# Kernel tuning notes

Measured on AMD Instinct MI355X. Metric: run time of the kernel, lower is better.

The kernel has to match this reference:

```python
import jax, jax.numpy as jnp
import numpy as np

B, M = 64, 2048
D_LLM = 4096
D_T, D_P, D_C = 256, 512, 1024
NH_T, NH_P, NH_C = 4, 8, 16
S_T, S_P, S_C = 4, 8, 4
LN_EPS = 1e-5


def setup_inputs() -> dict:
    key = jax.random.key(0)
    ks = iter(jax.random.split(key, 48))
    def n(shape, s=0.02):
        return jax.random.normal(next(ks), shape, jnp.float32) * s
    inp = {
        "hidden_state": jax.random.normal(next(ks), (B, D_LLM), jnp.float32),
        "time_fiber": jax.random.normal(next(ks), (M, D_T), jnp.float32),
        "topic_fiber": jax.random.normal(next(ks), (M, D_P), jnp.float32),
        "ctx_fiber": jax.random.normal(next(ks), (M, D_C), jnp.float32),
        "mem_mask": jnp.zeros((B, M), bool),
        # BundleQueryHeads: Linear(d_LLM -> d_F_*) per bundle (torch weight layout (out,in))
        "Wq_time": n((D_T, D_LLM)), "bq_time": jnp.zeros((D_T,), jnp.float32),
        "Wq_topic": n((D_P, D_LLM)), "bq_topic": jnp.zeros((D_P,), jnp.float32),
        "Wq_ctx": n((D_C, D_LLM)), "bq_ctx": jnp.zeros((D_C,), jnp.float32),
        # nn.MultiheadAttention packed in_proj (3d, d) and out_proj (d, d)
        "Wqkv_time": n((3 * D_T, D_T)), "bqkv_time": jnp.zeros((3 * D_T,), jnp.float32),
        "Wo_time": n((D_T, D_T)), "bo_time": jnp.zeros((D_T,), jnp.float32),
        "Wqkv_topic": n((3 * D_P, D_P)), "bqkv_topic": jnp.zeros((3 * D_P,), jnp.float32),
        "Wo_topic": n((D_P, D_P)), "bo_topic": jnp.zeros((D_P,), jnp.float32),
        "Wqkv_ctx": n((3 * D_C, D_C)), "bqkv_ctx": jnp.zeros((3 * D_C,), jnp.float32),
        "Wo_ctx": n((D_C, D_C)), "bo_ctx": jnp.zeros((D_C,), jnp.float32),
        # per-slot lifts stacked: (slots, d_F, d_LLM) for einsum 'bd,sde->bse'
        "Wlift_time": n((S_T, D_T, D_LLM)), "blift_time": jnp.zeros((S_T, D_LLM), jnp.float32),
        "Wlift_topic": n((S_P, D_P, D_LLM)), "blift_topic": jnp.zeros((S_P, D_LLM), jnp.float32),
        "Wlift_ctx": n((S_C, D_C, D_LLM)), "blift_ctx": jnp.zeros((S_C, D_LLM), jnp.float32),
        "ln_g": jnp.ones((D_LLM,), jnp.float32),
        "ln_b": jnp.zeros((D_LLM,), jnp.float32),
    }
    return inp


def _mha1(q, kv, Wqkv, bqkv, Wo, bo, nh, mask):
    """Single-query-token MHA. q: (B,d); kv: (M,d) shared across batch; mask: (B,M) True=ignore."""
    d = q.shape[-1]
    hd = d // nh
    Wq, Wk, Wv = jnp.split(Wqkv, 3, axis=0)
    bq, bk, bv = jnp.split(bqkv, 3, axis=0)
    qp = (q @ Wq.T + bq).reshape(-1, nh, hd)    # (B,h,hd)
    kp = (kv @ Wk.T + bk).reshape(-1, nh, hd)   # (M,h,hd)
    vp = (kv @ Wv.T + bv).reshape(-1, nh, hd)   # (M,h,hd)
    scale = 1.0 / np.float32(np.sqrt(hd))
    scores = jnp.einsum('bhd,mhd->bhm', qp, kp) * scale  # (B,h,M)
    scores = jnp.where(mask[:, None, :], jnp.float32(-1e9), scores)
    attn = jax.nn.softmax(scores, axis=-1)
    out = jnp.einsum('bhm,mhd->bhd', attn, vp).reshape(-1, d)  # (B,d)
    return out @ Wo.T + bo


def _layernorm(x, g, b):
    mu = jnp.mean(x, axis=-1, keepdims=True)
    var = jnp.mean((x - mu) ** 2, axis=-1, keepdims=True)
    return (x - mu) * jax.lax.rsqrt(var + LN_EPS) * g + b


def reference(hidden_state, time_fiber, topic_fiber, ctx_fiber, mem_mask,
              Wq_time, bq_time, Wq_topic, bq_topic, Wq_ctx, bq_ctx,
              Wqkv_time, bqkv_time, Wo_time, bo_time,
              Wqkv_topic, bqkv_topic, Wo_topic, bo_topic,
              Wqkv_ctx, bqkv_ctx, Wo_ctx, bo_ctx,
              Wlift_time, blift_time, Wlift_topic, blift_topic, Wlift_ctx, blift_ctx,
              ln_g, ln_b):
    # bundle query heads
    q_time = hidden_state @ Wq_time.T + bq_time
    q_topic = hidden_state @ Wq_topic.T + bq_topic
    q_ctx = hidden_state @ Wq_ctx.T + bq_ctx
    # three single-token cross attentions
    o_time = _mha1(q_time, time_fiber, Wqkv_time, bqkv_time, Wo_time, bo_time, NH_T, mem_mask)
    o_topic = _mha1(q_topic, topic_fiber, Wqkv_topic, bqkv_topic, Wo_topic, bo_topic, NH_P, mem_mask)
    o_ctx = _mha1(q_ctx, ctx_fiber, Wqkv_ctx, bqkv_ctx, Wo_ctx, bo_ctx, NH_C, mem_mask)
    # per-slot lifts, batched across slots
    slots_time = jnp.einsum('bd,sde->bse', o_time, Wlift_time) + blift_time[None]
    slots_topic = jnp.einsum('bd,sde->bse', o_topic, Wlift_topic) + blift_topic[None]
    slots_ctx = jnp.einsum('bd,sde->bse', o_ctx, Wlift_ctx) + blift_ctx[None]
    prefix = jnp.concatenate([slots_time, slots_topic, slots_ctx], axis=1)  # (B, L_mem, d_LLM)
    return _layernorm(prefix, ln_g, ln_b)
```

## Files before the change

kernel.cpp:

```cpp
#include <hip/hip_runtime.h>
#include <cstdint>
#include <cstddef>

typedef __attribute__((ext_vector_type(8))) short short8;
typedef __attribute__((ext_vector_type(4))) float floatx4;

__device__ __forceinline__ unsigned short f2bf(float f) {
    unsigned int u = __builtin_bit_cast(unsigned int, f);
    u += 0x7fffu + ((u >> 16) & 1u);
    return (unsigned short)(u >> 16);
}
__device__ __forceinline__ short8 pack8(float4 a, float4 b) {
    short8 r;
    r[0] = (short)f2bf(a.x); r[1] = (short)f2bf(a.y);
    r[2] = (short)f2bf(a.z); r[3] = (short)f2bf(a.w);
    r[4] = (short)f2bf(b.x); r[5] = (short)f2bf(b.y);
    r[6] = (short)f2bf(b.z); r[7] = (short)f2bf(b.w);
    return r;
}

struct WaveG {
    const float* A; const float* W; const float* bias; float* C;
    int K, Kc, ldw, ldc, nj, nkz, mode;
};
struct WaveBatch { WaveG d[16]; int start[16]; int nd; };

#define MFMA_ALL() { _Pragma("unroll") for (int r_ = 0; r_ < 4; ++r_) { \
    acc[r_][0] = __builtin_amdgcn_mfma_f32_16x16x32_bf16(af[r_], bfr0, acc[r_][0], 0, 0, 0); \
    acc[r_][1] = __builtin_amdgcn_mfma_f32_16x16x32_bf16(af[r_], bfr1, acc[r_][1], 0, 0, 0); } }

#define LOADA(dst) { _Pragma("unroll") for (int r_ = 0; r_ < 4; ++r_) { \
    dst[r_][0] = *(const float4*)pa[r_]; dst[r_][1] = *(const float4*)(pa[r_] + 4); \
    pa[r_] += 32; } }

#define PACKA(src) { _Pragma("unroll") for (int r_ = 0; r_ < 4; ++r_) \
    af[r_] = pack8(src[r_][0], src[r_][1]); }

__global__ __launch_bounds__(64) void wave_gemm(WaveBatch wb)
{
    const int bx = blockIdx.x;
    int di = 0;
#pragma unroll 1
    for (int i = 1; i < wb.nd; ++i) if (bx >= wb.start[i]) di = i;
    const WaveG g = wb.d[di];
    int local = bx - wb.start[di];
    const int j = local % g.nj;
    const int kz = local / g.nj;

    const int lane = threadIdx.x;
    const int quad = lane >> 4, l16 = lane & 15;

    const float* pa[4];
#pragma unroll
    for (int r = 0; r < 4; ++r)
        pa[r] = g.A + (size_t)(r * 16 + l16) * g.K + kz * g.Kc + quad * 8;

    floatx4 acc[4][2] = {};
    const int steps = g.Kc >> 5;
    short8 af[4], bfr0, bfr1;

    if (g.mode == 0) {
        const float* pb0 = g.W + (size_t)(j * 32 + l16) * g.K + kz * g.Kc + quad * 8;
        const float* pb1 = pb0 + (size_t)16 * g.K;
        float4 xa[4][2], ya[4][2];
        float4 xb[2][2], yb[2][2];
#define LOADB_NT(dst) { dst[0][0] = *(const float4*)pb0; dst[0][1] = *(const float4*)(pb0 + 4); \
        dst[1][0] = *(const float4*)pb1; dst[1][1] = *(const float4*)(pb1 + 4); \
        pb0 += 32; pb1 += 32; }
        LOADA(xa); LOADB_NT(xb);
        LOADA(ya); LOADB_NT(yb);
#pragma unroll 1
        for (int s = 0; s < steps; s += 2) {
            PACKA(xa);
            bfr0 = pack8(xb[0][0], xb[0][1]); bfr1 = pack8(xb[1][0], xb[1][1]);
            MFMA_ALL();
            if (s + 2 < steps) { LOADA(xa); LOADB_NT(xb); }
            PACKA(ya);
            bfr0 = pack8(yb[0][0], yb[0][1]); bfr1 = pack8(yb[1][0], yb[1][1]);
            MFMA_ALL();
            if (s + 3 < steps) { LOADA(ya); LOADB_NT(yb); }
        }
    } else {
        const float* pw[8];
#pragma unroll
        for (int i = 0; i < 8; ++i)
            pw[i] = g.W + ((size_t)(kz * g.Kc) + quad * 8 + i) * g.ldw + j * 32 + l16;
        const size_t ldw32 = (size_t)32 * g.ldw;
        float4 xa[4][2], ya[4][2];
        float xb[16], yb[16];
#define LOADB_NN(dst) { _Pragma("unroll") for (int i_ = 0; i_ < 8; ++i_) { \
        dst[i_] = pw[i_][0]; dst[8 + i_] = pw[i_][16]; pw[i_] += ldw32; } }
#define CVTB(src) { _Pragma("unroll") for (int e_ = 0; e_ < 8; ++e_) { \
        bfr0[e_] = (short)f2bf(src[e_]); bfr1[e_] = (short)f2bf(src[8 + e_]); } }
        LOADA(xa); LOADB_NN(xb);
        LOADA(ya); LOADB_NN(yb);
#pragma unroll 1
        for (int s = 0; s < steps; s += 2) {
            PACKA(xa);
            CVTB(xb);
            MFMA_ALL();
            if (s + 2 < steps) { LOADA(xa); LOADB_NN(xb); }
            PACKA(ya);
            CVTB(yb);
            MFMA_ALL();
            if (s + 3 < steps) { LOADA(ya); LOADB_NN(yb); }
        }
    }

#pragma unroll
    for (int r = 0; r < 4; ++r)
#pragma unroll
        for (int c = 0; c < 2; ++c) {
            const int col = j * 32 + c * 16 + l16;
            const float bj = (kz == 0) ? g.bias[col] : 0.f;
#pragma unroll
            for (int q = 0; q < 4; ++q) {
                const int row = r * 16 + quad * 4 + q;
                const float v = acc[r][c][q] + bj;
                if (g.nkz > 1) atomicAdd(&g.C[(size_t)row * g.ldc + col], v);
                else           g.C[(size_t)row * g.ldc + col] = v;
            }
        }
}

struct Sub128 { const float* A; const float* W; const float* bias; unsigned short* C; int K, N, nj; };
struct Batch128 { Sub128 d[4]; int start[4]; int nd; };

__global__ __launch_bounds__(256) void gemm128(Batch128 gb)
{
    __shared__ short As[2][128 * 40];
    __shared__ short Bs[2][128 * 40];

    const int bx = blockIdx.x;
    int di = 0;
#pragma unroll 1
    for (int i = 1; i < gb.nd; ++i) if (bx >= gb.start[i]) di = i;
    const Sub128 g = gb.d[di];
    const int local = bx - gb.start[di];
    const int jb = local % g.nj, ib = local / g.nj;

    const int tid = threadIdx.x;
    const int w = tid >> 6, lane = tid & 63;
    const int quad = lane >> 4, l16 = lane & 15;
    const int wm = (w >> 1) * 64, wn = (w & 1) * 64;

    const int rS = tid >> 1;
    const int gi0 = (tid & 1) * 2;
    const int jsw = (rS >> 3) & 3;
    const int s1 = rS * 40 + ((gi0 ^ jsw) << 3);
    const int s2 = rS * 40 + (((gi0 + 1) ^ jsw) << 3);
    const float* pa = g.A + (size_t)(ib * 128 + rS) * g.K + (tid & 1) * 16;
    const float* pb = g.W + (size_t)(jb * 128 + rS) * g.K + (tid & 1) * 16;

    int aoff[4], boff[4];
#pragma unroll
    for (int r = 0; r < 4; ++r) {
        int rowA = wm + r * 16 + l16;
        aoff[r] = rowA * 40 + ((quad ^ ((rowA >> 3) & 3)) << 3);
        int rowB = wn + r * 16 + l16;
        boff[r] = rowB * 40 + ((quad ^ ((rowB >> 3) & 3)) << 3);
    }

    floatx4 acc[4][4] = {};
    float4 a0 = *(const float4*)pa,       a1 = *(const float4*)(pa + 4);
    float4 a2 = *(const float4*)(pa + 8), a3 = *(const float4*)(pa + 12);
    float4 b0 = *(const float4*)pb,       b1 = *(const float4*)(pb + 4);
    float4 b2 = *(const float4*)(pb + 8), b3 = *(const float4*)(pb + 12);
    *(short8*)&As[0][s1] = pack8(a0, a1);
    *(short8*)&As[0][s2] = pack8(a2, a3);
    *(short8*)&Bs[0][s1] = pack8(b0, b1);
    *(short8*)&Bs[0][s2] = pack8(b2, b3);
    if (g.K > 32) {
        pa += 32; pb += 32;
        a0 = *(const float4*)pa;       a1 = *(const float4*)(pa + 4);
        a2 = *(const float4*)(pa + 8); a3 = *(const float4*)(pa + 12);
        b0 = *(const float4*)pb;       b1 = *(const float4*)(pb + 4);
        b2 = *(const float4*)(pb + 8); b3 = *(const float4*)(pb + 12);
    }
    int cur = 0;
#pragma unroll 1
    for (int k0 = 0; k0 < g.K; k0 += 32) {
        __syncthreads();
        short8 af[4], bf[4];
#pragma unroll
        for (int r = 0; r < 4; ++r) {
            af[r] = *(const short8*)&As[cur][aoff[r]];
            bf[r] = *(const short8*)&Bs[cur][boff[r]];
        }
#pragma unroll
        for (int r = 0; r < 4; ++r)
#pragma unroll
            for (int c = 0; c < 4; ++c)
                acc[r][c] = __builtin_amdgcn_mfma_f32_16x16x32_bf16(af[r], bf[c], acc[r][c], 0, 0, 0);
        if (k0 + 32 < g.K) {
            short* An = As[cur ^ 1]; short* Bn = Bs[cur ^ 1];
            *(short8*)&An[s1] = pack8(a0, a1);
            *(short8*)&An[s2] = pack8(a2, a3);
            *(short8*)&Bn[s1] = pack8(b0, b1);
            *(short8*)&Bn[s2] = pack8(b2, b3);
            if (k0 + 64 < g.K) {
                pa += 32; pb += 32;
                a0 = *(const float4*)pa;       a1 = *(const float4*)(pa + 4);
                a2 = *(const float4*)(pa + 8); a3 = *(const float4*)(pa + 12);
                b0 = *(const float4*)pb;       b1 = *(const float4*)(pb + 4);
                b2 = *(const float4*)(pb + 8); b3 = *(const float4*)(pb + 12);
            }
        }
        cur ^= 1;
    }

#pragma unroll
    for (int r = 0; r < 4; ++r)
#pragma unroll
        for (int c = 0; c < 4; ++c) {
            const int col = jb * 128 + wn + c * 16 + l16;
            const float bj = g.bias[col];
#pragma unroll
            for (int q = 0; q < 4; ++q) {
                const int row = ib * 128 + wm + r * 16 + quad * 4 + q;
                g.C[(size_t)row * g.N + col] = f2bf(acc[r][c][q] + bj);
            }
        }
}

__global__ __launch_bounds__(256) void qk_batch(
    const float* __restrict__ qp_t, const float* __restrict__ qp_p, const float* __restrict__ qp_c,
    const unsigned short* __restrict__ kv_t, const unsigned short* __restrict__ kv_p, const unsigned short* __restrict__ kv_c,
    float* __restrict__ S_t, float* __restrict__ S_p, float* __restrict__ S_c)
{
    __shared__ short As[64 * 72];
    __shared__ short Bs[128 * 72];
    const int hy = blockIdx.y;
    const float* qp; const unsigned short* kv; float* S; int d, h;
    if (hy < 4)       { qp = qp_t; kv = kv_t; S = S_t; d = 256;  h = hy; }
    else if (hy < 12) { qp = qp_p; kv = kv_p; S = S_p; d = 512;  h = hy - 4; }
    else              { qp = qp_c; kv = kv_c; S = S_c; d = 1024; h = hy - 12; }

    const int j0 = blockIdx.x * 128;
    const int tid = threadIdx.x;
    const int w = tid >> 6, lane = tid & 63;
    const int quad = lane >> 4, l16 = lane & 15;
    const int noff = w * 32;
    const int twoD = 2 * d;

    {
        const int b = tid >> 2, kc = (tid & 3) * 16;
        const float* ga = qp + (size_t)b * d + h * 64 + kc;
        float4 a0 = *(const float4*)(ga + 0), a1 = *(const float4*)(ga + 4);
        float4 a2 = *(const float4*)(ga + 8), a3 = *(const float4*)(ga + 12);
        *(short8*)&As[b * 72 + kc + 0] = pack8(a0, a1);
        *(short8*)&As[b * 72 + kc + 8] = pack8(a2, a3);
    }
    {
        const int m = tid >> 1, hf = (tid & 1) * 32;
        const unsigned short* gb = kv + (size_t)(j0 + m) * twoD + h * 64 + hf;
        uint4 b0 = *(const uint4*)(gb + 0),  b1 = *(const uint4*)(gb + 8);
        uint4 b2 = *(const uint4*)(gb + 16), b3 = *(const uint4*)(gb + 24);
        *(uint4*)&Bs[m * 72 + hf + 0]  = b0;
        *(uint4*)&Bs[m * 72 + hf + 8]  = b1;
        *(uint4*)&Bs[m * 72 + hf + 16] = b2;
        *(uint4*)&Bs[m * 72 + hf + 24] = b3;
    }
    __syncthreads();

    floatx4 acc[4][2] = {};
#pragma unroll
    for (int k0 = 0; k0 < 64; k0 += 32) {
        short8 af[4], bfr[2];
#pragma unroll
        for (int r = 0; r < 4; ++r)
            af[r] = *(const short8*)&As[(r * 16 + l16) * 72 + k0 + quad * 8];
#pragma unroll
        for (int c = 0; c < 2; ++c)
            bfr[c] = *(const short8*)&Bs[(noff + c * 16 + l16) * 72 + k0 + quad * 8];
#pragma unroll
        for (int r = 0; r < 4; ++r)
#pragma unroll
            for (int c = 0; c < 2; ++c)
                acc[r][c] = __builtin_amdgcn_mfma_f32_16x16x32_bf16(af[r], bfr[c], acc[r][c], 0, 0, 0);
    }
#pragma unroll
    for (int r = 0; r < 4; ++r)
#pragma unroll
        for (int c = 0; c < 2; ++c) {
            int col = j0 + noff + c * 16 + l16;
#pragma unroll
            for (int q = 0; q < 4; ++q) {
                int row = r * 16 + quad * 4 + q;
                S[((size_t)h * 64 + row) * 2048 + col] = acc[r][c][q] * 0.125f;
            }
        }
}

__global__ __launch_bounds__(256) void softmax_p(
    float* __restrict__ S_t, float* __restrict__ S_p, float* __restrict__ S_c,
    const uint8_t* __restrict__ mask)
{
    const int hy = blockIdx.x, b = blockIdx.y;
    float* S; int h;
    if (hy < 4)       { S = S_t; h = hy; }
    else if (hy < 12) { S = S_p; h = hy - 4; }
    else              { S = S_c; h = hy - 12; }

    const int tid = threadIdx.x;
    __shared__ __align__(16) float sc[2048];
    __shared__ float red[4];
    __shared__ float s_max, s_sum;

    float* Sr = S + ((size_t)h * 64 + b) * 2048;
    const uint8_t* mr = mask + (size_t)b * 2048;

    float lmax = -1e30f;
    for (int m = tid; m < 2048; m += 256) {
        float s = Sr[m];
        if (mr[m]) s = -1e9f;
        sc[m] = s;
        lmax = fmaxf(lmax, s);
    }
#pragma unroll
    for (int off = 32; off; off >>= 1) lmax = fmaxf(lmax, __shfl_down(lmax, off));
    if ((tid & 63) == 0) red[tid >> 6] = lmax;
    __syncthreads();
    if (tid == 0) s_max = fmaxf(fmaxf(red[0], red[1]), fmaxf(red[2], red[3]));
    __syncthreads();
    const float mx = s_max;

    float lsum = 0.f;
    for (int m = tid; m < 2048; m += 256) {
        float e = __expf(sc[m] - mx);
        sc[m] = e;
        lsum += e;
    }
#pragma unroll
    for (int off = 32; off; off >>= 1) lsum += __shfl_down(lsum, off);
    if ((tid & 63) == 0) red[tid >> 6] = lsum;
    __syncthreads();
    if (tid == 0) s_sum = red[0] + red[1] + red[2] + red[3];
    __syncthreads();
    const float inv = 1.f / s_sum;

    for (int m = tid; m < 2048; m += 256) Sr[m] = sc[m] * inv;
}

__global__ __launch_bounds__(64) void pv_batch(
    const float* __restrict__ P_t, const float* __restrict__ P_p, const float* __restrict__ P_c,
    const unsigned short* __restrict__ kv_t, const unsigned short* __restrict__ kv_p, const unsigned short* __restrict__ kv_c,
    float* __restrict__ o_t, float* __restrict__ o_p, float* __restrict__ o_c)
{
    const int hy = blockIdx.x, kz = blockIdx.y;
    const float* P; const unsigned short* kv; float* o; int d, h;
    if (hy < 4)       { P = P_t; kv = kv_t; o = o_t; d = 256;  h = hy; }
    else if (hy < 12) { P = P_p; kv = kv_p; o = o_p; d = 512;  h = hy - 4; }
    else              { P = P_c; kv = kv_c; o = o_c; d = 1024; h = hy - 12; }

    const int lane = threadIdx.x;
    const int quad = lane >> 4, l16 = lane & 15;
    const int twoD = 2 * d;

    const float* pa[4];
#pragma unroll
    for (int r = 0; r < 4; ++r)
        pa[r] = P + ((size_t)h * 64 + r * 16 + l16) * 2048 + kz * 128 + quad * 8;
    const unsigned short* pb = kv + (size_t)(kz * 128 + quad * 8) * twoD + d + h * 64 + l16;

    floatx4 acc[4][4] = {};
#pragma unroll 1
    for (int s = 0; s < 4; ++s) {
        short8 af[4];
#pragma unroll
        for (int r = 0; r < 4; ++r) {
            float4 a0 = *(const float4*)pa[r], a1 = *(const float4*)(pa[r] + 4);
            af[r] = pack8(a0, a1);
            pa[r] += 32;
        }
        short8 bf[4];
#pragma unroll
        for (int c = 0; c < 4; ++c)
#pragma unroll
            for (int i = 0; i < 8; ++i)
                bf[c][i] = (short)pb[(size_t)i * twoD + c * 16];
        pb += (size_t)32 * twoD;
#pragma unroll
        for (int r = 0; r < 4; ++r)
#pragma unroll
            for (int c = 0; c < 4; ++c)
                acc[r][c] = __builtin_amdgcn_mfma_f32_16x16x32_bf16(af[r], bf[c], acc[r][c], 0, 0, 0);
    }
#pragma unroll
    for (int r = 0; r < 4; ++r)
#pragma unroll
        for (int c = 0; c < 4; ++c)
#pragma unroll
            for (int q = 0; q < 4; ++q) {
                const int row = r * 16 + quad * 4 + q;
                atomicAdd(&o[(size_t)row * d + h * 64 + c * 16 + l16], acc[r][c][q]);
            }
}

__global__ __launch_bounds__(256) void ln_kernel(
    float* __restrict__ x, const float* __restrict__ g, const float* __restrict__ bb)
{
    const int row = blockIdx.x;
    float* xr = x + (size_t)row * 4096;
    const int tid = threadIdx.x;
    float v[16];
    float sum = 0.f, sumsq = 0.f;
#pragma unroll
    for (int i = 0; i < 16; ++i) {
        v[i] = xr[tid + i * 256];
        sum += v[i];
        sumsq += v[i] * v[i];
    }
    __shared__ float rs[4], rq[4];
#pragma unroll
    for (int off = 32; off; off >>= 1) {
        sum += __shfl_down(sum, off);
        sumsq += __shfl_down(sumsq, off);
    }
    if ((tid & 63) == 0) { rs[tid >> 6] = sum; rq[tid >> 6] = sumsq; }
    __syncthreads();
    const float ts = rs[0] + rs[1] + rs[2] + rs[3];
    const float tq = rq[0] + rq[1] + rq[2] + rq[3];
    const float mu = ts * (1.f / 4096.f);
    const float var = tq * (1.f / 4096.f) - mu * mu;
    const float r = rsqrtf(var + 1e-5f);
#pragma unroll
    for (int i = 0; i < 16; ++i) {
        int e = tid + i * 256;
        xr[e] = (v[i] - mu) * r * g[e] + bb[e];
    }
}

static void addw(WaveBatch& G, int& tot,
                 const float* A, const float* W, const float* bias, float* C,
                 int K, int Kc, int ldw, int ldc, int nj, int nkz, int mode)
{
    WaveG& s = G.d[G.nd];
    s.A = A; s.W = W; s.bias = bias; s.C = C;
    s.K = K; s.Kc = Kc; s.ldw = ldw; s.ldc = ldc; s.nj = nj; s.nkz = nkz; s.mode = mode;
    G.start[G.nd] = tot;
    tot += nj * nkz;
    G.nd++;
}
static void add128(Batch128& G, int& tot,
                   const float* A, const float* W, const float* bias, unsigned short* C,
                   int K, int N, int nj, int ni)
{
    Sub128& s = G.d[G.nd];
    s.A = A; s.W = W; s.bias = bias; s.C = C; s.K = K; s.N = N; s.nj = nj;
    G.start[G.nd] = tot;
    tot += nj * ni;
    G.nd++;
}

extern "C" void kernel_launch(void* const* d_in, const int* in_sizes, int n_in,
                              void* d_out, int out_size, void* d_ws, size_t ws_size,
                              hipStream_t stream)
{
    const float*   hs     = (const float*)d_in[0];
    const float*   fib_t  = (const float*)d_in[1];
    const float*   fib_p  = (const float*)d_in[2];
    const float*   fib_c  = (const float*)d_in[3];
    const uint8_t* mask   = (const uint8_t*)d_in[4];
    const float* Wq_t   = (const float*)d_in[5];  const float* bq_t   = (const float*)d_in[6];
    const float* Wq_p   = (const float*)d_in[7];  const float* bq_p   = (const float*)d_in[8];
    const float* Wq_c   = (const float*)d_in[9];  const float* bq_c   = (const float*)d_in[10];
    const float* Wqkv_t = (const float*)d_in[11]; const float* bqkv_t = (const float*)d_in[12];
    const float* Wo_t   = (const float*)d_in[13]; const float* bo_t   = (const float*)d_in[14];
    const float* Wqkv_p = (const float*)d_in[15]; const float* bqkv_p = (const float*)d_in[16];
    const float* Wo_p   = (const float*)d_in[17]; const float* bo_p   = (const float*)d_in[18];
    const float* Wqkv_c = (const float*)d_in[19]; const float* bqkv_c = (const float*)d_in[20];
    const float* Wo_c   = (const float*)d_in[21]; const float* bo_c   = (const float*)d_in[22];
    const float* Wl_t   = (const float*)d_in[23]; const float* bl_t   = (const float*)d_in[24];
    const float* Wl_p   = (const float*)d_in[25]; const float* bl_p   = (const float*)d_in[26];
    const float* Wl_c   = (const float*)d_in[27]; const float* bl_c   = (const float*)d_in[28];
    const float* ln_g   = (const float*)d_in[29]; const float* ln_b   = (const float*)d_in[30];

    char* wsb = (char*)d_ws;
    float* q_t  = (float*)wsb; wsb += 64 * 256 * 4;
    float* q_p  = (float*)wsb; wsb += 64 * 512 * 4;
    float* q_c  = (float*)wsb; wsb += 64 * 1024 * 4;
    float* qp_t = (float*)wsb; wsb += 64 * 256 * 4;
    float* qp_p = (float*)wsb; wsb += 64 * 512 * 4;
    float* qp_c = (float*)wsb; wsb += 64 * 1024 * 4;
    float* po_t = (float*)wsb; wsb += 64 * 256 * 4;
    float* po_p = (float*)wsb; wsb += 64 * 512 * 4;
    float* po_c = (float*)wsb; wsb += 64 * 1024 * 4;
    float* o_t  = (float*)wsb; wsb += 64 * 256 * 4;
    float* o_p  = (float*)wsb; wsb += 64 * 512 * 4;
    float* o_c  = (float*)wsb; wsb += 64 * 1024 * 4;
    size_t zbytes = (size_t)(wsb - (char*)d_ws);
    unsigned short* kv_t = (unsigned short*)wsb; wsb += 2048 * 512 * 2;
    unsigned short* kv_p = (unsigned short*)wsb; wsb += 2048 * 1024 * 2;
    unsigned short* kv_c = (unsigned short*)wsb; wsb += 2048 * 2048 * 2;
    float* S_t = (float*)wsb; wsb += (size_t)4  * 64 * 2048 * 4;
    float* S_p = (float*)wsb; wsb += (size_t)8  * 64 * 2048 * 4;
    float* S_c = (float*)wsb; wsb += (size_t)16 * 64 * 2048 * 4;
    float* out = (float*)d_out;

    hipMemsetAsync(d_ws, 0, zbytes, stream);
    hipMemsetAsync(d_out, 0, (size_t)out_size, stream);

    {
        WaveBatch G{}; int tot = 0; G.nd = 0;
        addw(G, tot, hs, Wq_c, bq_c, q_c, 4096, 128, 0, 1024, 32, 32, 0);
        addw(G, tot, hs, Wq_p, bq_p, q_p, 4096, 128, 0, 512,  16, 32, 0);
        addw(G, tot, hs, Wq_t, bq_t, q_t, 4096, 128, 0, 256,  8,  32, 0);
        wave_gemm<<<dim3(tot), dim3(64), 0, stream>>>(G);
    }

    {
        Batch128 G{}; int tot = 0; G.nd = 0;
        add128(G, tot, fib_c, Wqkv_c + 1024 * 1024, bqkv_c + 1024, kv_c, 1024, 2048, 16, 16);
        add128(G, tot, fib_p, Wqkv_p + 512 * 512,   bqkv_p + 512,  kv_p, 512,  1024, 8,  16);
        add128(G, tot, fib_t, Wqkv_t + 256 * 256,   bqkv_t + 256,  kv_t, 256,  512,  4,  16);
        gemm128<<<dim3(tot), dim3(256), 0, stream>>>(G);
    }

    {
        WaveBatch G{}; int tot = 0; G.nd = 0;
        addw(G, tot, q_c, Wqkv_c, bqkv_c, qp_c, 1024, 128, 0, 1024, 32, 8, 0);
        addw(G, tot, q_p, Wqkv_p, bqkv_p, qp_p, 512,  128, 0, 512,  16, 4, 0);
        addw(G, tot, q_t, Wqkv_t, bqkv_t, qp_t, 256,  128, 0, 256,  8,  2, 0);
        wave_gemm<<<dim3(tot), dim3(64), 0, stream>>>(G);
    }

    qk_batch<<<dim3(16, 28), dim3(256), 0, stream>>>(qp_t, qp_p, qp_c, kv_t, kv_p, kv_c, S_t, S_p, S_c);
    softmax_p<<<dim3(28, 64), dim3(256), 0, stream>>>(S_t, S_p, S_c, mask);
    pv_batch<<<dim3(28, 16), dim3(64), 0, stream>>>(S_t, S_p, S_c, kv_t, kv_p, kv_c, o_t, o_p, o_c);

    {
        WaveBatch G{}; int tot = 0; G.nd = 0;
        addw(G, tot, o_c, Wo_c, bo_c, po_c, 1024, 128, 0, 1024, 32, 8, 0);
        addw(G, tot, o_p, Wo_p, bo_p, po_p, 512,  128, 0, 512,  16, 4, 0);
        addw(G, tot, o_t, Wo_t, bo_t, po_t, 256,  128, 0, 256,  8,  2, 0);
        wave_gemm<<<dim3(tot), dim3(64), 0, stream>>>(G);
    }

    {
        WaveBatch G{}; int tot = 0; G.nd = 0;
        for (int z = 0; z < 4; ++z)
            addw(G, tot, po_c, Wl_c + (size_t)z * 1024 * 4096, bl_c + z * 4096,
                 out + (size_t)(12 + z) * 4096, 1024, 256, 4096, 16 * 4096, 128, 4, 1);
        for (int z = 0; z < 8; ++z)
            addw(G, tot, po_p, Wl_p + (size_t)z * 512 * 4096, bl_p + z * 4096,
                 out + (size_t)(4 + z) * 4096, 512, 256, 4096, 16 * 4096, 128, 2, 1);
        for (int z = 0; z < 4; ++z)
            addw(G, tot, po_t, Wl_t + (size_t)z * 256 * 4096, bl_t + z * 4096,
                 out + (size_t)z * 4096, 256, 256, 4096, 16 * 4096, 128, 1, 1);
        wave_gemm<<<dim3(tot), dim3(64), 0, stream>>>(G);
    }

    ln_kernel<<<dim3(1024), dim3(256), 0, stream>>>(out, ln_g, ln_b);
}
```

Baseline: 396.3 us.

## Stage wave_gemm tiles through LDS with coalesced loads and double buffering

The single-wave GEMM now loads A and B tiles with coalesced row-contiguous float4 reads, converts them to bf16, and stores them into double-buffered shared memory. MFMA fragments are then read from LDS. The aim is to avoid the strided, poorly coalesced global reads of the old direct-to-register path, especially the scalar column loads in the transposed (mode 1) weight path. In exchange it adds LDS traffic, scalar transposed LDS stores in mode 1 that may cause bank conflicts, and relies on the single wave for ordering since there are no barriers. It also sets a min-blocks hint of 4 in launch_bounds.

```diff
diff --git a/kernel.cpp b/kernel.cpp
--- a/kernel.cpp
+++ b/kernel.cpp
@@ -3,6 +3,7 @@
 #include <cstddef>
 
 typedef __attribute__((ext_vector_type(8))) short short8;
+typedef __attribute__((ext_vector_type(4))) short short4v;
 typedef __attribute__((ext_vector_type(4))) float floatx4;
 
 __device__ __forceinline__ unsigned short f2bf(float f) {
@@ -18,6 +19,12 @@
     r[6] = (short)f2bf(b.z); r[7] = (short)f2bf(b.w);
     return r;
 }
+__device__ __forceinline__ short4v pack4(float4 a) {
+    short4v r;
+    r[0] = (short)f2bf(a.x); r[1] = (short)f2bf(a.y);
+    r[2] = (short)f2bf(a.z); r[3] = (short)f2bf(a.w);
+    return r;
+}
 
 struct WaveG {
     const float* A; const float* W; const float* bias; float* C;
@@ -25,19 +32,11 @@
 };
 struct WaveBatch { WaveG d[16]; int start[16]; int nd; };
 
-#define MFMA_ALL() { _Pragma("unroll") for (int r_ = 0; r_ < 4; ++r_) { \
-    acc[r_][0] = __builtin_amdgcn_mfma_f32_16x16x32_bf16(af[r_], bfr0, acc[r_][0], 0, 0, 0); \
-    acc[r_][1] = __builtin_amdgcn_mfma_f32_16x16x32_bf16(af[r_], bfr1, acc[r_][1], 0, 0, 0); } }
-
-#define LOADA(dst) { _Pragma("unroll") for (int r_ = 0; r_ < 4; ++r_) { \
-    dst[r_][0] = *(const float4*)pa[r_]; dst[r_][1] = *(const float4*)(pa[r_] + 4); \
-    pa[r_] += 32; } }
-
-#define PACKA(src) { _Pragma("unroll") for (int r_ = 0; r_ < 4; ++r_) \
-    af[r_] = pack8(src[r_][0], src[r_][1]); }
-
-__global__ __launch_bounds__(64) void wave_gemm(WaveBatch wb)
-{
+__global__ __launch_bounds__(64, 4) void wave_gemm(WaveBatch wb)
+{
+    __shared__ __align__(16) short Abuf[2][64 * 40];
+    __shared__ __align__(16) short Bbuf[2][32 * 40];
+
     const int bx = blockIdx.x;
     int di = 0;
 #pragma unroll 1
@@ -49,62 +48,72 @@
 
     const int lane = threadIdx.x;
     const int quad = lane >> 4, l16 = lane & 15;
-
-    const float* pa[4];
-#pragma unroll
-    for (int r = 0; r < 4; ++r)
-        pa[r] = g.A + (size_t)(r * 16 + l16) * g.K + kz * g.Kc + quad * 8;
+    const int ldr  = lane >> 3;
+    const int ldc4 = (lane & 7) * 4;
+
+    const float* pa = g.A + (size_t)ldr * g.K + kz * g.Kc + ldc4;
+    const float* pb;
+    size_t pbstep;
+    size_t pbpass;
+    if (g.mode == 0) {
+        pb = g.W + (size_t)(j * 32 + ldr) * g.K + kz * g.Kc + ldc4;
+        pbstep = 32; pbpass = (size_t)8 * g.K;
+    } else {
+        pb = g.W + ((size_t)(kz * g.Kc) + ldr) * g.ldw + j * 32 + ldc4;
+        pbstep = (size_t)32 * g.ldw; pbpass = (size_t)8 * g.ldw;
+    }
+    const size_t papass = (size_t)8 * g.K;
+
+    const int steps = g.Kc >> 5;
+
+    float4 ra[8], rb[4];
+
+#define LOADSTEP(soff) { \
+    _Pragma("unroll") for (int p_ = 0; p_ < 8; ++p_) \
+        ra[p_] = *(const float4*)(pa + (soff) * 32 + p_ * papass); \
+    _Pragma("unroll") for (int p_ = 0; p_ < 4; ++p_) \
+        rb[p_] = *(const float4*)(pb + (soff) * pbstep + p_ * pbpass); }
+
+#define STORESTEP(buf) { \
+    _Pragma("unroll") for (int p_ = 0; p_ < 8; ++p_) \
+        *(short4v*)&Abuf[buf][(p_ * 8 + ldr) * 40 + ldc4] = pack4(ra[p_]); \
+    if (g.mode == 0) { \
+        _Pragma("unroll") for (int p_ = 0; p_ < 4; ++p_) \
+            *(short4v*)&Bbuf[buf][(p_ * 8 + ldr) * 40 + ldc4] = pack4(rb[p_]); \
+    } else { \
+        _Pragma("unroll") for (int p_ = 0; p_ < 4; ++p_) { \
+            const int krow_ = p_ * 8 + ldr; \
+            Bbuf[buf][(ldc4 + 0) * 40 + krow_] = (short)f2bf(rb[p_].x); \
+            Bbuf[buf][(ldc4 + 1) * 40 + krow_] = (short)f2bf(rb[p_].y); \
+            Bbuf[buf][(ldc4 + 2) * 40 + krow_] = (short)f2bf(rb[p_].z); \
+            Bbuf[buf][(ldc4 + 3) * 40 + krow_] = (short)f2bf(rb[p_].w); \
+        } } }
 
     floatx4 acc[4][2] = {};
-    const int steps = g.Kc >> 5;
-    short8 af[4], bfr0, bfr1;
-
-    if (g.mode == 0) {
-        const float* pb0 = g.W + (size_t)(j * 32 + l16) * g.K + kz * g.Kc + quad * 8;
-        const float* pb1 = pb0 + (size_t)16 * g.K;
-        float4 xa[4][2], ya[4][2];
-        float4 xb[2][2], yb[2][2];
-#define LOADB_NT(dst) { dst[0][0] = *(const float4*)pb0; dst[0][1] = *(const float4*)(pb0 + 4); \
-        dst[1][0] = *(const float4*)pb1; dst[1][1] = *(const float4*)(pb1 + 4); \
-        pb0 += 32; pb1 += 32; }
-        LOADA(xa); LOADB_NT(xb);
-        LOADA(ya); LOADB_NT(yb);
+
+    LOADSTEP(0);
+    STORESTEP(0);
+    if (steps > 1) LOADSTEP(1);
+
+    int cur = 0;
 #pragma unroll 1
-        for (int s = 0; s < steps; s += 2) {
-            PACKA(xa);
-            bfr0 = pack8(xb[0][0], xb[0][1]); bfr1 = pack8(xb[1][0], xb[1][1]);
-            MFMA_ALL();
-            if (s + 2 < steps) { LOADA(xa); LOADB_NT(xb); }
-            PACKA(ya);
-            bfr0 = pack8(yb[0][0], yb[0][1]); bfr1 = pack8(yb[1][0], yb[1][1]);
-            MFMA_ALL();
-            if (s + 3 < steps) { LOADA(ya); LOADB_NT(yb); }
-        }
-    } else {
-        const float* pw[8];
-#pragma unroll
-        for (int i = 0; i < 8; ++i)
-            pw[i] = g.W + ((size_t)(kz * g.Kc) + quad * 8 + i) * g.ldw + j * 32 + l16;
-        const size_t ldw32 = (size_t)32 * g.ldw;
-        float4 xa[4][2], ya[4][2];
-        float xb[16], yb[16];
-#define LOADB_NN(dst) { _Pragma("unroll") for (int i_ = 0; i_ < 8; ++i_) { \
-        dst[i_] = pw[i_][0]; dst[8 + i_] = pw[i_][16]; pw[i_] += ldw32; } }
-#define CVTB(src) { _Pragma("unroll") for (int e_ = 0; e_ < 8; ++e_) { \
-        bfr0[e_] = (short)f2bf(src[e_]); bfr1[e_] = (short)f2bf(src[8 + e_]); } }
-        LOADA(xa); LOADB_NN(xb);
-        LOADA(ya); LOADB_NN(yb);
-#pragma unroll 1
-        for (int s = 0; s < steps; s += 2) {
-            PACKA(xa);
-            CVTB(xb);
-            MFMA_ALL();
-            if (s + 2 < steps) { LOADA(xa); LOADB_NN(xb); }
-            PACKA(ya);
-            CVTB(yb);
-            MFMA_ALL();
-            if (s + 3 < steps) { LOADA(ya); LOADB_NN(yb); }
-        }
+    for (int s = 0; s < steps; ++s) {
+        short8 af[4], bfr0, bfr1;
+#pragma unroll
+        for (int r = 0; r < 4; ++r)
+            af[r] = *(const short8*)&Abuf[cur][(r * 16 + l16) * 40 + quad * 8];
+        bfr0 = *(const short8*)&Bbuf[cur][(l16) * 40 + quad * 8];
+        bfr1 = *(const short8*)&Bbuf[cur][(16 + l16) * 40 + quad * 8];
+#pragma unroll
+        for (int r = 0; r < 4; ++r) {
+            acc[r][0] = __builtin_amdgcn_mfma_f32_16x16x32_bf16(af[r], bfr0, acc[r][0], 0, 0, 0);
+            acc[r][1] = __builtin_amdgcn_mfma_f32_16x16x32_bf16(af[r], bfr1, acc[r][1], 0, 0, 0);
+        }
+        if (s + 1 < steps) {
+            STORESTEP(cur ^ 1);
+            if (s + 2 < steps) LOADSTEP(s + 2);
+        }
+        cur ^= 1;
     }
 
 #pragma unroll
@@ -121,6 +130,8 @@
                 else           g.C[(size_t)row * g.ldc + col] = v;
             }
         }
+#undef LOADSTEP
+#undef STORESTEP
 }
 
 struct Sub128 { const float* A; const float* W; const float* bias; unsigned short* C; int K, N, nj; };
```

After: 392.6 us. Within noise of the previous version (-0.9%).
